# Optimization experiments

Hardware: AMD Instinct MI355X
Metric: run time of the kernel (lower is better)

Reference implementation:

```python
import jax, jax.numpy as jnp
import numpy as np
from jax import lax

STRIDES = (8, 16, 32, 64, 128)
LEVEL_HW = ((100, 128), (50, 64), (25, 32), (13, 16), (7, 8))
NUM_CLASSES = 80
PRE_NMS_THRESH = 0.05
PRE_NMS_TOPK = 1000
NMS_THRESH = 0.6
MAX_DET = 100
CLS_OFFSET = 1.0e4  # > max image coordinate, separates classes for joint NMS


def setup_inputs() -> dict:
    key = jax.random.key(0)
    B = 16
    ks = jax.random.split(key, 3 * len(LEVEL_HW))
    inp = {}
    i = 0
    for lvl, (h, w) in enumerate(LEVEL_HW):
        # shift logits down so sigmoid scores are mostly below the 0.05 candidate
        # threshold (realistic detection sparsity)
        inp[f"logits_p{lvl + 3}"] = jax.random.normal(ks[i], (B, NUM_CLASSES, h, w), jnp.float32) - 4.0; i += 1
        inp[f"bbox_p{lvl + 3}"] = jax.random.uniform(ks[i], (B, 4, h, w), jnp.float32, minval=0.0, maxval=64.0); i += 1
        inp[f"ctr_p{lvl + 3}"] = jax.random.normal(ks[i], (B, 1, h, w), jnp.float32); i += 1
    inp["im_info"] = jnp.tile(jnp.array([[800.0, 1024.0]], jnp.float32), (B, 1))
    return inp


def _locations(h, w, stride):
    # FCOSLocation: center of each stride cell -> [HW, 2] as (x, y)
    sx = jnp.arange(w, dtype=jnp.float32) * stride + stride // 2
    sy = jnp.arange(h, dtype=jnp.float32) * stride + stride // 2
    yy, xx = jnp.meshgrid(sy, sx, indexing="ij")
    return jnp.stack([xx.reshape(-1), yy.reshape(-1)], axis=-1)


def _nms_single(boxes, scores, classes):
    # boxes [K,4], scores [K] (descending), classes [K] int
    off = classes.astype(jnp.float32)[:, None] * CLS_OFFSET
    nb = boxes + off  # class-offset trick -> per-class NMS in one pass
    areas = jnp.maximum(nb[:, 2] - nb[:, 0], 0.0) * jnp.maximum(nb[:, 3] - nb[:, 1], 0.0)

    def body(sc, _):
        i = jnp.argmax(sc)
        s = sc[i]
        bi = nb[i]
        xx1 = jnp.maximum(bi[0], nb[:, 0])
        yy1 = jnp.maximum(bi[1], nb[:, 1])
        xx2 = jnp.minimum(bi[2], nb[:, 2])
        yy2 = jnp.minimum(bi[3], nb[:, 3])
        inter = jnp.maximum(xx2 - xx1, 0.0) * jnp.maximum(yy2 - yy1, 0.0)
        iou = inter / (areas[i] + areas - inter + 1e-9)
        sc2 = jnp.where(iou >= NMS_THRESH, -jnp.inf, sc).at[i].set(-jnp.inf)
        return sc2, (i, s > 0.0)

    _, (idxs, valid) = lax.scan(body, scores, None, length=MAX_DET)
    det = jnp.concatenate(
        [boxes[idxs], scores[idxs][:, None], classes[idxs].astype(jnp.float32)[:, None]],
        axis=-1,
    )  # [MAX_DET, 6] = x1,y1,x2,y2,score,class
    return jnp.where(valid[:, None], det, 0.0)


def _forward(logits_p3, bbox_p3, ctr_p3, logits_p4, bbox_p4, ctr_p4,
             logits_p5, bbox_p5, ctr_p5, logits_p6, bbox_p6, ctr_p6,
             logits_p7, bbox_p7, ctr_p7, im_info):
    levels = [(logits_p3, bbox_p3, ctr_p3), (logits_p4, bbox_p4, ctr_p4),
              (logits_p5, bbox_p5, ctr_p5), (logits_p6, bbox_p6, ctr_p6),
              (logits_p7, bbox_p7, ctr_p7)]
    scores_l, boxes_l = [], []
    for (lg, rg, ct), stride in zip(levels, STRIDES):
        B, C, H, W = lg.shape
        cls = jax.nn.sigmoid(lg).transpose(0, 2, 3, 1).reshape(B, H * W, C)
        cen = jax.nn.sigmoid(ct).transpose(0, 2, 3, 1).reshape(B, H * W, 1)
        # candidate threshold on raw class prob, then modulate by centerness
        comb = jnp.where(cls > PRE_NMS_THRESH, cls * cen, 0.0)
        locs = _locations(H, W, stride)  # [HW, 2]
        reg = rg.transpose(0, 2, 3, 1).reshape(B, H * W, 4)  # (l, t, r, b)
        bx = jnp.stack([locs[None, :, 0] - reg[..., 0],
                        locs[None, :, 1] - reg[..., 1],
                        locs[None, :, 0] + reg[..., 2],
                        locs[None, :, 1] + reg[..., 3]], axis=-1)
        scores_l.append(comb)
        boxes_l.append(bx)
    scores = jnp.concatenate(scores_l, axis=1)  # [B, N, C]
    boxes = jnp.concatenate(boxes_l, axis=1)    # [B, N, 4]
    B, N, C = scores.shape
    vals, idx = lax.top_k(scores.reshape(B, N * C), PRE_NMS_TOPK)  # [B, K]
    loc = idx // C
    cls_id = idx % C
    cand = jnp.take_along_axis(boxes, loc[..., None], axis=1)  # [B, K, 4]
    h = im_info[:, 0:1]
    w = im_info[:, 1:2]
    x1 = jnp.clip(cand[..., 0], 0.0, w - 1.0)
    y1 = jnp.clip(cand[..., 1], 0.0, h - 1.0)
    x2 = jnp.clip(cand[..., 2], 0.0, w - 1.0)
    y2 = jnp.clip(cand[..., 3], 0.0, h - 1.0)
    cand = jnp.stack([x1, y1, x2, y2], axis=-1)
    sc = jnp.where(vals > 0.0, jnp.sqrt(jnp.maximum(vals, 0.0) + 1e-12), 0.0)
    return jax.vmap(_nms_single)(cand, sc, cls_id)  # [B, MAX_DET, 6]


def reference(logits_p3, bbox_p3, ctr_p3, logits_p4, bbox_p4, ctr_p4,
              logits_p5, bbox_p5, ctr_p5, logits_p6, bbox_p6, ctr_p6,
              logits_p7, bbox_p7, ctr_p7, im_info):
    return _forward(logits_p3, bbox_p3, ctr_p3, logits_p4, bbox_p4, ctr_p4,
                    logits_p5, bbox_p5, ctr_p5, logits_p6, bbox_p6, ctr_p6,
                    logits_p7, bbox_p7, ctr_p7, im_info)
```

## Files before the change

kernel.cpp:

```cpp
#include <hip/hip_runtime.h>
#include <math.h>

#pragma clang fp contract(off)

#define NB 16
#define NC 80
#define NTOT 17064
#define TOPK 1000
#define NBINS 8192
#define CAP 4096
#define MAXDET 100
#define NREP 4
#define CNTSTRIDE 64
#define CHUNK 128
#define G1 128
#define NSEG 512
#define SEGW 512

struct Ptrs {
    const float* lg[5];
    const float* bb[5];
    const float* ct[5];
};

__device__ __forceinline__ void level_of(int n, int& l, int& hw, int& W,
                                         int& stride, int& half, int& HW) {
    if (n < 12800)      { l = 0; hw = n;         W = 128; stride = 8;   half = 4;  HW = 12800; }
    else if (n < 16000) { l = 1; hw = n - 12800; W = 64;  stride = 16;  half = 8;  HW = 3200;  }
    else if (n < 16800) { l = 2; hw = n - 16000; W = 32;  stride = 32;  half = 16; HW = 800;   }
    else if (n < 17008) { l = 3; hw = n - 16800; W = 16;  stride = 64;  half = 32; HW = 208;   }
    else                { l = 4; hw = n - 17008; W = 8;   stride = 128; half = 64; HW = 56;    }
}

__device__ __forceinline__ float fast_sig(float x) {
    float e = __expf(-x);
    return __builtin_amdgcn_rcpf(1.0f + e);
}

template<int HW4, int NF4, int LVOFF>
__device__ __forceinline__ void scan_level(const float* lgb, const float* ctb,
        int tid, int lane, int bx, int gx, unsigned FB_LO,
        unsigned long long* segp, unsigned& cur, unsigned long long ltmask) {
    for (int i0 = bx * 256; i0 < NF4; i0 += gx * 256) {
        int i = i0 + tid;
        bool f0 = false, f1 = false, f2 = false, f3 = false;
        unsigned long long k0 = 0, k1 = 0, k2 = 0, k3 = 0;
        if (i < NF4) {
            int c   = i / HW4;
            int hwf = i - c * HW4;
            float4 v = *(const float4*)(lgb + c * (HW4 * 4) + hwf * 4);
            if (v.x > -2.47f || v.y > -2.47f || v.z > -2.47f || v.w > -2.47f) {
                float4 cv = *(const float4*)(ctb + hwf * 4);
                int nbase = LVOFF + hwf * 4;
#define DO_J(J, X, CT, F, K)                                                  \
                if ((X) > -2.47f) {                                           \
                    float cls = fast_sig(X);                                  \
                    float cen = fast_sig(CT);                                 \
                    unsigned bits = __float_as_uint(cls * cen);               \
                    if (bits >= FB_LO) {                                      \
                        unsigned idx = (unsigned)((nbase + (J)) * NC + c);    \
                        K = ((unsigned long long)bits << 32) |                \
                            (0xFFFFFFFFu - idx);                              \
                        F = true;                                             \
                    }                                                         \
                }
                DO_J(0, v.x, cv.x, f0, k0)
                DO_J(1, v.y, cv.y, f1, k1)
                DO_J(2, v.z, cv.z, f2, k2)
                DO_J(3, v.w, cv.w, f3, k3)
#undef DO_J
            }
        }
        unsigned long long m0 = __ballot(f0), m1 = __ballot(f1);
        unsigned long long m2 = __ballot(f2), m3 = __ballot(f3);
        if ((m0 | m1 | m2 | m3) == 0ULL) continue;
        unsigned t0 = (unsigned)__popcll(m0), t1 = (unsigned)__popcll(m1);
        unsigned t2 = (unsigned)__popcll(m2), t3 = (unsigned)__popcll(m3);
        if (f0) { unsigned pos = cur + (unsigned)__popcll(m0 & ltmask);                if (pos < SEGW) segp[pos] = k0; }
        if (f1) { unsigned pos = cur + t0 + (unsigned)__popcll(m1 & ltmask);           if (pos < SEGW) segp[pos] = k1; }
        if (f2) { unsigned pos = cur + t0 + t1 + (unsigned)__popcll(m2 & ltmask);      if (pos < SEGW) segp[pos] = k2; }
        if (f3) { unsigned pos = cur + t0 + t1 + t2 + (unsigned)__popcll(m3 & ltmask); if (pos < SEGW) segp[pos] = k3; }
        cur += t0 + t1 + t2 + t3;
    }
}

__global__ void __launch_bounds__(256) k_scoreF(Ptrs p, unsigned* segcnt,
                                                unsigned long long* segbuf,
                                                unsigned* cnt2) {
    int b = blockIdx.y, tid = threadIdx.x, bx = blockIdx.x, gx = gridDim.x;
    int lane = tid & 63, wv = tid >> 6;
    if (bx == 0 && tid == 0) cnt2[(size_t)b * CNTSTRIDE] = 0;
    unsigned long long ltmask = (1ULL << lane) - 1ULL;
    unsigned FB_LO = __float_as_uint(0.08f) - 64u;
    unsigned long long* segp = segbuf + (((size_t)b * G1 + bx) * 4 + wv) * SEGW;
    unsigned cur = 0;

    scan_level<3200, 256000,     0>(p.lg[0] + (size_t)b * NC * 12800, p.ct[0] + (size_t)b * 12800, tid, lane, bx, gx, FB_LO, segp, cur, ltmask);
    scan_level< 800,  64000, 12800>(p.lg[1] + (size_t)b * NC * 3200,  p.ct[1] + (size_t)b * 3200,  tid, lane, bx, gx, FB_LO, segp, cur, ltmask);
    scan_level< 200,  16000, 16000>(p.lg[2] + (size_t)b * NC * 800,   p.ct[2] + (size_t)b * 800,   tid, lane, bx, gx, FB_LO, segp, cur, ltmask);
    scan_level<  52,   4160, 16800>(p.lg[3] + (size_t)b * NC * 208,   p.ct[3] + (size_t)b * 208,   tid, lane, bx, gx, FB_LO, segp, cur, ltmask);
    scan_level<  14,   1120, 17008>(p.lg[4] + (size_t)b * NC * 56,    p.ct[4] + (size_t)b * 56,    tid, lane, bx, gx, FB_LO, segp, cur, ltmask);

    if (lane == 0) segcnt[(size_t)b * NSEG + bx * 4 + wv] = cur;
}

template<int HW4, int NF4>
__device__ __forceinline__ void histf_level(const float* lgb, const float* ctb,
                                            int tid, unsigned* hist) {
    for (int i0 = 0; i0 < NF4; i0 += 1024) {
        int i = i0 + tid;
        if (i < NF4) {
            int c   = i / HW4;
            int hwf = i - c * HW4;
            float4 v = *(const float4*)(lgb + c * (HW4 * 4) + hwf * 4);
            if (v.x > -2.95f || v.y > -2.95f || v.z > -2.95f || v.w > -2.95f) {
                float4 cv = *(const float4*)(ctb + hwf * 4);
                float xs[4] = {v.x, v.y, v.z, v.w};
                float cs[4] = {cv.x, cv.y, cv.z, cv.w};
#pragma unroll
                for (int j = 0; j < 4; ++j) {
                    float x = xs[j];
                    if (x > -2.95f) {
                        float cls = fast_sig(x);
                        if (cls > 0.04999f) {
                            bool in = true;
                            if (cls < 0.05001f)
                                in = (1.0f / (1.0f + expf(-x))) > 0.05f;
                            if (in) {
                                float cen = fast_sig(cs[j]);
                                unsigned bits = __float_as_uint(cls * cen);
                                unsigned cb = (bits > 32u) ? bits - 32u : 0u;
                                atomicAdd(&hist[cb >> 19], 1u);
                            }
                        }
                    }
                }
            }
        }
    }
}

__global__ void __launch_bounds__(1024) k_threshF(Ptrs p, const unsigned* segcnt,
                                                  const unsigned long long* segbuf,
                                                  unsigned* T, unsigned* okf) {
    __shared__ unsigned hist[NBINS];
    __shared__ unsigned wred[16], wtot[16];
    __shared__ int s_flags;
    __shared__ int Tf;
    int b = blockIdx.x, tid = threadIdx.x, lane = tid & 63, wv = tid >> 6;
    if (tid == 0) { s_flags = 0; Tf = 0; }
    for (int i = tid; i < NBINS; i += 1024) hist[i] = 0;
    __syncthreads();

    bool ovf = false;
    for (int sg = wv; sg < NSEG; sg += 16) {
        unsigned cnt = segcnt[(size_t)b * NSEG + sg];
        if (cnt > SEGW) { ovf = true; cnt = SEGW; }
        const unsigned long long* src = segbuf + ((size_t)b * NSEG + sg) * SEGW;
        for (int i = lane; i < (int)cnt; i += 64) {
            unsigned bits = (unsigned)(src[i] >> 32);
            unsigned cb = (bits > 32u) ? bits - 32u : 0u;
            atomicAdd(&hist[cb >> 19], 1u);
        }
    }
    if (ovf) atomicOr(&s_flags, 1);
    __syncthreads();

    const unsigned B0 = __float_as_uint(0.08f);
    const int OKBIN = (int)(B0 >> 19) + 1;
    int base = tid * 8;
    unsigned okp = 0;
#pragma unroll
    for (int i = 0; i < 8; ++i) if (base + i >= OKBIN) okp += hist[base + i];
    for (int off = 32; off > 0; off >>= 1) okp += __shfl_down(okp, off);
    if (lane == 0) wred[wv] = okp;
    __syncthreads();
    if (tid == 0) {
        unsigned tot = 0;
        for (int w = 0; w < 16; ++w) tot += wred[w];
        if ((s_flags & 1) || tot < TOPK) atomicOr(&s_flags, 2);
    }
    __syncthreads();

    if (s_flags & 2) {
        for (int i = tid; i < NBINS; i += 1024) hist[i] = 0;
        __syncthreads();
        histf_level<3200, 256000>(p.lg[0] + (size_t)b * NC * 12800, p.ct[0] + (size_t)b * 12800, tid, hist);
        histf_level< 800,  64000>(p.lg[1] + (size_t)b * NC * 3200,  p.ct[1] + (size_t)b * 3200,  tid, hist);
        histf_level< 200,  16000>(p.lg[2] + (size_t)b * NC * 800,   p.ct[2] + (size_t)b * 800,   tid, hist);
        histf_level<  52,   4160>(p.lg[3] + (size_t)b * NC * 208,   p.ct[3] + (size_t)b * 208,   tid, hist);
        histf_level<  14,   1120>(p.lg[4] + (size_t)b * NC * 56,    p.ct[4] + (size_t)b * 56,    tid, hist);
        __syncthreads();
    }

    unsigned mysum = 0;
#pragma unroll
    for (int i = 0; i < 8; ++i) mysum += hist[base + i];
    unsigned incl = mysum;
#pragma unroll
    for (int off = 1; off < 64; off <<= 1) {
        unsigned v = __shfl_down(incl, off);
        if (lane + off < 64) incl += v;
    }
    if (lane == 0) wtot[wv] = incl;
    __syncthreads();
    unsigned above = 0;
    for (int w = wv + 1; w < 16; ++w) above += wtot[w];
    unsigned sufincl = incl + above;
    unsigned excl = sufincl - mysum;
    if (excl < TOPK && sufincl >= TOPK) {
        unsigned running = excl;
        for (int bin = base + 7; bin >= base; --bin) {
            running += hist[bin];
            if (running >= TOPK) { Tf = bin; break; }
        }
    }
    __syncthreads();
    if (tid == 0) { T[b] = (unsigned)Tf; okf[b] = (s_flags & 2) ? 0u : 1u; }
}

template<int HW4, int NF4, int LVOFF>
__device__ __forceinline__ void compact_level(const float* lgb, const float* ctb,
        int tid, int lane, int bx, int gx, unsigned Tb, float xpre,
        unsigned* cntb, unsigned long long* selb, unsigned long long ltmask) {
    for (int i0 = bx * 256; i0 < NF4; i0 += gx * 256) {
        int i = i0 + tid;
        bool f0 = false, f1 = false, f2 = false, f3 = false;
        unsigned long long k0 = 0, k1 = 0, k2 = 0, k3 = 0;
        if (i < NF4) {
            int c   = i / HW4;
            int hwf = i - c * HW4;
            float4 v = *(const float4*)(lgb + c * (HW4 * 4) + hwf * 4);
            if (v.x > xpre || v.y > xpre || v.z > xpre || v.w > xpre) {
                float4 cv = *(const float4*)(ctb + hwf * 4);
                int nbase = LVOFF + hwf * 4;
#define DO_J(J, X, CT, F, K)                                                  \
                if ((X) > xpre) {                                             \
                    float cls = 1.0f / (1.0f + expf(-(X)));                   \
                    if (cls > 0.05f) {                                        \
                        float cen = 1.0f / (1.0f + expf(-(CT)));              \
                        float comb = cls * cen;                               \
                        unsigned bits = __float_as_uint(comb);                \
                        if ((bits >> 19) >= Tb) {                             \
                            unsigned idx = (unsigned)((nbase + (J)) * NC + c);\
                            K = ((unsigned long long)bits << 32) |            \
                                (0xFFFFFFFFu - idx);                          \
                            F = true;                                         \
                        }                                                     \
                    }                                                         \
                }
                DO_J(0, v.x, cv.x, f0, k0)
                DO_J(1, v.y, cv.y, f1, k1)
                DO_J(2, v.z, cv.z, f2, k2)
                DO_J(3, v.w, cv.w, f3, k3)
#undef DO_J
            }
        }
        unsigned long long m0 = __ballot(f0), m1 = __ballot(f1);
        unsigned long long m2 = __ballot(f2), m3 = __ballot(f3);
        if ((m0 | m1 | m2 | m3) == 0ULL) continue;
        unsigned t0 = (unsigned)__popcll(m0), t1 = (unsigned)__popcll(m1);
        unsigned t2 = (unsigned)__popcll(m2), t3 = (unsigned)__popcll(m3);
        unsigned total = t0 + t1 + t2 + t3;
        int basep = 0;
        if (lane == 0) basep = (int)atomicAdd(cntb, total);
        basep = __shfl(basep, 0);
        if (f0) { int pos = basep + (int)__popcll(m0 & ltmask);                       if (pos < CAP) selb[pos] = k0; }
        if (f1) { int pos = basep + (int)t0 + (int)__popcll(m1 & ltmask);             if (pos < CAP) selb[pos] = k1; }
        if (f2) { int pos = basep + (int)(t0 + t1) + (int)__popcll(m2 & ltmask);      if (pos < CAP) selb[pos] = k2; }
        if (f3) { int pos = basep + (int)(t0 + t1 + t2) + (int)__popcll(m3 & ltmask); if (pos < CAP) selb[pos] = k3; }
    }
}

__global__ void __launch_bounds__(256) k_filterF(Ptrs p, const unsigned* T,
                                                 const unsigned* okf,
                                                 const unsigned* segcnt,
                                                 const unsigned long long* segbuf,
                                                 unsigned* cnt2, unsigned long long* sel) {
    int b = blockIdx.y, tid = threadIdx.x, lane = tid & 63;
    int bx = blockIdx.x, gx = gridDim.x;
    unsigned Tb = T[b];
    unsigned long long ltmask = (1ULL << lane) - 1ULL;
    unsigned* cntb = cnt2 + (size_t)b * CNTSTRIDE;
    unsigned long long* selb = sel + (size_t)b * CAP;

    if (okf[b]) {
        unsigned Tshift = Tb << 19;
        unsigned fmin = (Tshift >= 32u) ? Tshift - 32u : 0u;
        int per = NSEG / gx;
        for (int sg = bx * per; sg < bx * per + per; ++sg) {
            unsigned sc = segcnt[(size_t)b * NSEG + sg];
            if (sc > SEGW) sc = SEGW;
            const unsigned long long* src = segbuf + ((size_t)b * NSEG + sg) * SEGW;
            for (int i = tid; i < (int)sc; i += 256) {
                unsigned long long e = src[i];
                bool f = false;
                unsigned long long key = 0;
                if ((unsigned)(e >> 32) >= fmin) {
                    unsigned idx = 0xFFFFFFFFu - (unsigned)(e & 0xFFFFFFFFu);
                    int n = idx / NC, c = idx - n * NC;
                    int l, hw, W, stride, half, HW;
                    level_of(n, l, hw, W, stride, half, HW);
                    float x  = p.lg[l][(size_t)b * NC * HW + (size_t)c * HW + hw];
                    float ct = p.ct[l][(size_t)b * HW + hw];
                    float cls = 1.0f / (1.0f + expf(-x));
                    if (cls > 0.05f) {
                        float cen = 1.0f / (1.0f + expf(-ct));
                        unsigned be = __float_as_uint(cls * cen);
                        if ((be >> 19) >= Tb) {
                            key = ((unsigned long long)be << 32) | (e & 0xFFFFFFFFULL);
                            f = true;
                        }
                    }
                }
                unsigned long long mk = __ballot(f);
                if (mk) {
                    unsigned nw = (unsigned)__popcll(mk);
                    int basep = 0;
                    if (lane == 0) basep = (int)atomicAdd(cntb, nw);
                    basep = __shfl(basep, 0);
                    if (f) {
                        int pos = basep + (int)__popcll(mk & ltmask);
                        if (pos < CAP) selb[pos] = key;
                    }
                }
            }
        }
    } else {
        float mthr = __uint_as_float(Tb << 19);
        float xpre = -2.95f;
        if (mthr > 1e-37f && mthr < 1.0f) {
            float lm = logf(mthr / (1.0f - mthr)) - 0.01f;
            if (lm > xpre) xpre = lm;
        }
        compact_level<3200, 256000,     0>(p.lg[0] + (size_t)b * NC * 12800, p.ct[0] + (size_t)b * 12800, tid, lane, bx, gx, Tb, xpre, cntb, selb, ltmask);
        compact_level< 800,  64000, 12800>(p.lg[1] + (size_t)b * NC * 3200,  p.ct[1] + (size_t)b * 3200,  tid, lane, bx, gx, Tb, xpre, cntb, selb, ltmask);
        compact_level< 200,  16000, 16000>(p.lg[2] + (size_t)b * NC * 800,   p.ct[2] + (size_t)b * 800,   tid, lane, bx, gx, Tb, xpre, cntb, selb, ltmask);
        compact_level<  52,   4160, 16800>(p.lg[3] + (size_t)b * NC * 208,   p.ct[3] + (size_t)b * 208,   tid, lane, bx, gx, Tb, xpre, cntb, selb, ltmask);
        compact_level<  14,   1120, 17008>(p.lg[4] + (size_t)b * NC * 56,    p.ct[4] + (size_t)b * 56,    tid, lane, bx, gx, Tb, xpre, cntb, selb, ltmask);
    }
}

template<int HW4, int NF4>
__device__ __forceinline__ void hist_level(const float* lgb, const float* ctb,
                                           int tid, int bx, int gx, unsigned* lh) {
    for (int i0 = bx * 256; i0 < NF4; i0 += gx * 256) {
        int i = i0 + tid;
        if (i < NF4) {
            int c   = i / HW4;
            int hwf = i - c * HW4;
            float4 v  = *(const float4*)(lgb + c * (HW4 * 4) + hwf * 4);
            if (v.x > -2.95f || v.y > -2.95f || v.z > -2.95f || v.w > -2.95f) {
                float4 cv = *(const float4*)(ctb + hwf * 4);
                float xs[4] = {v.x, v.y, v.z, v.w};
                float cs[4] = {cv.x, cv.y, cv.z, cv.w};
#pragma unroll
                for (int j = 0; j < 4; ++j) {
                    float x = xs[j];
                    if (x > -2.95f) {
                        float cls = fast_sig(x);
                        if (cls > 0.04999f) {
                            bool in = true;
                            if (cls < 0.05001f)
                                in = (1.0f / (1.0f + expf(-x))) > 0.05f;
                            if (in) {
                                float cen = fast_sig(cs[j]);
                                unsigned bits = __float_as_uint(cls * cen);
                                unsigned cb = (bits > 32u) ? bits - 32u : 0u;
                                atomicAdd(&lh[cb >> 19], 1u);
                            }
                        }
                    }
                }
            }
        }
    }
}

__global__ void __launch_bounds__(256) k_histA(Ptrs p, unsigned* hist) {
    __shared__ unsigned lh[NBINS];
    int b = blockIdx.y, tid = threadIdx.x, bx = blockIdx.x, gx = gridDim.x;
    for (int i = tid; i < NBINS; i += 256) lh[i] = 0;
    __syncthreads();
    hist_level<3200, 256000>(p.lg[0] + (size_t)b * NC * 12800, p.ct[0] + (size_t)b * 12800, tid, bx, gx, lh);
    hist_level< 800,  64000>(p.lg[1] + (size_t)b * NC * 3200,  p.ct[1] + (size_t)b * 3200,  tid, bx, gx, lh);
    hist_level< 200,  16000>(p.lg[2] + (size_t)b * NC * 800,   p.ct[2] + (size_t)b * 800,   tid, bx, gx, lh);
    hist_level<  52,   4160>(p.lg[3] + (size_t)b * NC * 208,   p.ct[3] + (size_t)b * 208,   tid, bx, gx, lh);
    hist_level<  14,   1120>(p.lg[4] + (size_t)b * NC * 56,    p.ct[4] + (size_t)b * 56,    tid, bx, gx, lh);
    __syncthreads();
    unsigned* h = hist + ((size_t)(bx & (NREP - 1)) * NB + b) * NBINS;
    for (int i = tid; i < NBINS; i += 256) {
        unsigned v = lh[i];
        if (v) atomicAdd(&h[i], v);
    }
}

__global__ void __launch_bounds__(256) k_thresh(const unsigned* hist, unsigned* T) {
    __shared__ unsigned hl[NBINS];
    __shared__ unsigned wtot[4];
    __shared__ int Tf;
    int b = blockIdx.x, tid = threadIdx.x, lane = tid & 63, wv = tid >> 6;
    if (tid == 0) Tf = 0;
    for (int i = tid; i < NBINS; i += 256) {
        unsigned s = 0;
        for (int r = 0; r < NREP; ++r)
            s += hist[((size_t)r * NB + b) * NBINS + i];
        hl[i] = s;
    }
    __syncthreads();
    int base = tid * 32;
    unsigned mysum = 0;
#pragma unroll
    for (int i = 0; i < 32; ++i) mysum += hl[base + i];
    unsigned incl = mysum;
#pragma unroll
    for (int off = 1; off < 64; off <<= 1) {
        unsigned v = __shfl_down(incl, off);
        if (lane + off < 64) incl += v;
    }
    if (lane == 0) wtot[wv] = incl;
    __syncthreads();
    unsigned above = 0;
    for (int w = wv + 1; w < 4; ++w) above += wtot[w];
    unsigned sufincl = incl + above;
    unsigned excl = sufincl - mysum;
    if (excl < TOPK && sufincl >= TOPK) {
        unsigned running = excl;
        for (int bin = base + 31; bin >= base; --bin) {
            running += hl[bin];
            if (running >= TOPK) { Tf = bin; break; }
        }
    }
    __syncthreads();
    if (tid == 0) T[b] = (unsigned)Tf;
}

__global__ void __launch_bounds__(256) k_compactB(Ptrs p, const unsigned* T,
                                                  unsigned* cnt2, unsigned long long* sel) {
    int b = blockIdx.y, tid = threadIdx.x, lane = tid & 63;
    int bx = blockIdx.x, gx = gridDim.x;
    unsigned Tb = T[b];
    float mthr = __uint_as_float(Tb << 19);
    float xpre = -2.95f;
    if (mthr > 1e-37f && mthr < 1.0f) {
        float lm = logf(mthr / (1.0f - mthr)) - 0.01f;
        if (lm > xpre) xpre = lm;
    }
    unsigned long long ltmask = (1ULL << lane) - 1ULL;
    unsigned* cntb = cnt2 + (size_t)b * CNTSTRIDE;
    unsigned long long* selb = sel + (size_t)b * CAP;
    compact_level<3200, 256000,     0>(p.lg[0] + (size_t)b * NC * 12800, p.ct[0] + (size_t)b * 12800, tid, lane, bx, gx, Tb, xpre, cntb, selb, ltmask);
    compact_level< 800,  64000, 12800>(p.lg[1] + (size_t)b * NC * 3200,  p.ct[1] + (size_t)b * 3200,  tid, lane, bx, gx, Tb, xpre, cntb, selb, ltmask);
    compact_level< 200,  16000, 16000>(p.lg[2] + (size_t)b * NC * 800,   p.ct[2] + (size_t)b * 800,   tid, lane, bx, gx, Tb, xpre, cntb, selb, ltmask);
    compact_level<  52,   4160, 16800>(p.lg[3] + (size_t)b * NC * 208,   p.ct[3] + (size_t)b * 208,   tid, lane, bx, gx, Tb, xpre, cntb, selb, ltmask);
    compact_level<  14,   1120, 17008>(p.lg[4] + (size_t)b * NC * 56,    p.ct[4] + (size_t)b * 56,    tid, lane, bx, gx, Tb, xpre, cntb, selb, ltmask);
}

__global__ void __launch_bounds__(256) k_rankdec(Ptrs p, const unsigned* cnt,
                                                 const unsigned long long* sel,
                                                 const float* im_info, float* cand) {
    __shared__ __align__(16) unsigned long long keys[CAP];
    int b = blockIdx.y, tid = threadIdx.x;
    unsigned M = cnt[(size_t)b * CNTSTRIDE];
    if (M > CAP) M = CAP;
    int s0 = blockIdx.x * 256;
    if (s0 >= (int)M) return;
    int Mpad = (int)((M + 1u) & ~1u);
    for (int i = tid; i < Mpad; i += 256)
        keys[i] = (i < (int)M) ? sel[(size_t)b * CAP + i] : 0ULL;
    __syncthreads();

    int s = s0 + tid;
    if (s >= (int)M) return;
    unsigned long long k = keys[s];
    int rank = 0;
    for (int j = 0; j < Mpad; j += 2) {
        ulonglong2 kk = *(const ulonglong2*)&keys[j];
        rank += (kk.x > k) ? 1 : 0;
        rank += (kk.y > k) ? 1 : 0;
    }
    if (rank >= TOPK) return;

    float Him = im_info[b * 2 + 0], Wim = im_info[b * 2 + 1];
    float xmax = Wim - 1.0f, ymax = Him - 1.0f;
    unsigned sb = (unsigned)(k >> 32);
    unsigned idx = 0xFFFFFFFFu - (unsigned)(k & 0xFFFFFFFFu);
    float val = __uint_as_float(sb);
    int n = idx / NC, c = idx - n * NC;
    int l, hw, W, stride, half, HW;
    level_of(n, l, hw, W, stride, half, HW);
    int wx = hw % W, hy = hw / W;
    float locx = (float)(wx * stride + half);
    float locy = (float)(hy * stride + half);
    const float* bb = p.bb[l] + (size_t)b * 4 * HW + hw;
    float r0 = bb[0], r1 = bb[(size_t)HW], r2 = bb[(size_t)2 * HW], r3 = bb[(size_t)3 * HW];
    float x1 = locx - r0, y1 = locy - r1, x2 = locx + r2, y2 = locy + r3;
    x1 = fminf(fmaxf(x1, 0.f), xmax);
    y1 = fminf(fmaxf(y1, 0.f), ymax);
    x2 = fminf(fmaxf(x2, 0.f), xmax);
    y2 = fminf(fmaxf(y2, 0.f), ymax);
    float scv = sqrtf(val + 1e-12f);
    float off = (float)c * 10000.0f;
    float a0 = x1 + off, a1 = y1 + off, a2 = x2 + off, a3 = y2 + off;
    float area = fmaxf(a2 - a0, 0.f) * fmaxf(a3 - a1, 0.f);
    float* dst = cand + ((size_t)b * TOPK + rank) * 12;
    *(float4*)(dst + 0) = make_float4(x1, y1, x2, y2);
    *(float4*)(dst + 4) = make_float4(a0, a1, a2, a3);
    *(float4*)(dst + 8) = make_float4(area, scv, (float)c, 0.f);
}

__global__ void __launch_bounds__(64) k_nms(const unsigned* cnt, const float* cand,
                                            float* out) {
    __shared__ float4 s_ob[CHUNK], s_nb[CHUNK], s_ms[CHUNK];
    int b = blockIdx.x, lane = threadIdx.x;
    unsigned M = cnt[(size_t)b * CNTSTRIDE];
    if (M > CAP) M = CAP;
    int ncand = (int)M < TOPK ? (int)M : TOPK;
    const float* src = cand + (size_t)b * TOPK * 12;
    float* ob = out + (size_t)b * MAXDET * 6;

    int na = 0;
    float4 a0b = make_float4(0.f, 0.f, 0.f, 0.f);
    float4 a1b = make_float4(0.f, 0.f, 0.f, 0.f);
    float a0a = 0.f, a1a = 0.f;

    for (int base = 0; base < ncand && na < MAXDET; base += CHUNK) {
        int cn = ncand - base; if (cn > CHUNK) cn = CHUNK;
        for (int cidx = lane; cidx < cn; cidx += 64) {
            const float* s = src + (size_t)(base + cidx) * 12;
            s_ob[cidx] = *(const float4*)(s + 0);
            s_nb[cidx] = *(const float4*)(s + 4);
            s_ms[cidx] = *(const float4*)(s + 8);
        }
        __syncthreads();
        for (int r = 0; r < cn && na < MAXDET; ++r) {
            float4 cb = s_nb[r];
            float ca = s_ms[r].x;
            bool sup = false;
            if (lane < na) {
                float xx1 = fmaxf(a0b.x, cb.x);
                float yy1 = fmaxf(a0b.y, cb.y);
                float xx2 = fminf(a0b.z, cb.z);
                float yy2 = fminf(a0b.w, cb.w);
                float inter = fmaxf(xx2 - xx1, 0.f) * fmaxf(yy2 - yy1, 0.f);
                float iou = inter / (((a0a + ca) - inter) + 1e-9f);
                sup = (iou >= 0.6f);
            }
            if (lane + 64 < na) {
                float xx1 = fmaxf(a1b.x, cb.x);
                float yy1 = fmaxf(a1b.y, cb.y);
                float xx2 = fminf(a1b.z, cb.z);
                float yy2 = fminf(a1b.w, cb.w);
                float inter = fmaxf(xx2 - xx1, 0.f) * fmaxf(yy2 - yy1, 0.f);
                float iou = inter / (((a1a + ca) - inter) + 1e-9f);
                sup |= (iou >= 0.6f);
            }
            if (__ballot(sup) == 0ULL) {
                if (lane == (na & 63)) {
                    if (na < 64) { a0b = cb; a0a = ca; }
                    else         { a1b = cb; a1a = ca; }
                }
                if (lane == 0) {
                    float4 o4 = s_ob[r]; float4 m4 = s_ms[r];
                    ob[na * 6 + 0] = o4.x; ob[na * 6 + 1] = o4.y;
                    ob[na * 6 + 2] = o4.z; ob[na * 6 + 3] = o4.w;
                    ob[na * 6 + 4] = m4.y; ob[na * 6 + 5] = m4.z;
                }
                ++na;
            }
        }
        __syncthreads();
    }
    for (int q = na * 6 + lane; q < MAXDET * 6; q += 64)
        ob[q] = 0.f;
}

extern "C" void kernel_launch(void* const* d_in, const int* in_sizes, int n_in,
                              void* d_out, int out_size, void* d_ws, size_t ws_size,
                              hipStream_t stream) {
    Ptrs p;
    for (int l = 0; l < 5; ++l) {
        p.lg[l] = (const float*)d_in[3 * l + 0];
        p.bb[l] = (const float*)d_in[3 * l + 1];
        p.ct[l] = (const float*)d_in[3 * l + 2];
    }
    const float* im_info = (const float*)d_in[15];
    float* out = (float*)d_out;
    unsigned char* w = (unsigned char*)d_ws;

    if (ws_size >= (size_t)34884096) {
        unsigned* segcnt           = (unsigned*)(w);
        unsigned* cnt2             = (unsigned*)(w + 32768);
        unsigned* T                = (unsigned*)(w + 36864);
        unsigned* okf              = (unsigned*)(w + 37120);
        unsigned long long* sel    = (unsigned long long*)(w + 37376);
        float* cand                = (float*)(w + 561664);
        unsigned long long* segbuf = (unsigned long long*)(w + 1329664);

        k_scoreF<<<dim3(G1, NB), 256, 0, stream>>>(p, segcnt, segbuf, cnt2);
        k_threshF<<<NB, 1024, 0, stream>>>(p, segcnt, segbuf, T, okf);
        k_filterF<<<dim3(32, NB), 256, 0, stream>>>(p, T, okf, segcnt, segbuf, cnt2, sel);
        k_rankdec<<<dim3(16, NB), 256, 0, stream>>>(p, cnt2, sel, im_info, cand);
        k_nms<<<NB, 64, 0, stream>>>(cnt2, cand, out);
    } else {
        unsigned* hist          = (unsigned*)(w);
        unsigned* cnt2          = (unsigned*)(w + 2097152);
        unsigned* T             = (unsigned*)(w + 2101248);
        unsigned long long* sel = (unsigned long long*)(w + 2101504);
        float* cand             = (float*)(w + 2625792);

        hipMemsetAsync(w, 0, 2101504, stream);
        k_histA<<<dim3(64, NB), 256, 0, stream>>>(p, hist);
        k_thresh<<<NB, 256, 0, stream>>>(hist, T);
        k_compactB<<<dim3(128, NB), 256, 0, stream>>>(p, T, cnt2, sel);
        k_rankdec<<<dim3(16, NB), 256, 0, stream>>>(p, cnt2, sel, im_info, cand);
        k_nms<<<NB, 64, 0, stream>>>(cnt2, cand, out);
    }
}
```

Baseline: 277.1 us.

## Fuse threshold and filter kernels into single per-image pick kernel

```diff
diff --git a/kernel.cpp b/kernel.cpp
--- a/kernel.cpp
+++ b/kernel.cpp
@@ -85,11 +85,9 @@
 }
 
 __global__ void __launch_bounds__(256) k_scoreF(Ptrs p, unsigned* segcnt,
-                                                unsigned long long* segbuf,
-                                                unsigned* cnt2) {
+                                                unsigned long long* segbuf) {
     int b = blockIdx.y, tid = threadIdx.x, bx = blockIdx.x, gx = gridDim.x;
     int lane = tid & 63, wv = tid >> 6;
-    if (bx == 0 && tid == 0) cnt2[(size_t)b * CNTSTRIDE] = 0;
     unsigned long long ltmask = (1ULL << lane) - 1ULL;
     unsigned FB_LO = __float_as_uint(0.08f) - 64u;
     unsigned long long* segp = segbuf + (((size_t)b * G1 + bx) * 4 + wv) * SEGW;
@@ -140,85 +138,6 @@
     }
 }
 
-__global__ void __launch_bounds__(1024) k_threshF(Ptrs p, const unsigned* segcnt,
-                                                  const unsigned long long* segbuf,
-                                                  unsigned* T, unsigned* okf) {
-    __shared__ unsigned hist[NBINS];
-    __shared__ unsigned wred[16], wtot[16];
-    __shared__ int s_flags;
-    __shared__ int Tf;
-    int b = blockIdx.x, tid = threadIdx.x, lane = tid & 63, wv = tid >> 6;
-    if (tid == 0) { s_flags = 0; Tf = 0; }
-    for (int i = tid; i < NBINS; i += 1024) hist[i] = 0;
-    __syncthreads();
-
-    bool ovf = false;
-    for (int sg = wv; sg < NSEG; sg += 16) {
-        unsigned cnt = segcnt[(size_t)b * NSEG + sg];
-        if (cnt > SEGW) { ovf = true; cnt = SEGW; }
-        const unsigned long long* src = segbuf + ((size_t)b * NSEG + sg) * SEGW;
-        for (int i = lane; i < (int)cnt; i += 64) {
-            unsigned bits = (unsigned)(src[i] >> 32);
-            unsigned cb = (bits > 32u) ? bits - 32u : 0u;
-            atomicAdd(&hist[cb >> 19], 1u);
-        }
-    }
-    if (ovf) atomicOr(&s_flags, 1);
-    __syncthreads();
-
-    const unsigned B0 = __float_as_uint(0.08f);
-    const int OKBIN = (int)(B0 >> 19) + 1;
-    int base = tid * 8;
-    unsigned okp = 0;
-#pragma unroll
-    for (int i = 0; i < 8; ++i) if (base + i >= OKBIN) okp += hist[base + i];
-    for (int off = 32; off > 0; off >>= 1) okp += __shfl_down(okp, off);
-    if (lane == 0) wred[wv] = okp;
-    __syncthreads();
-    if (tid == 0) {
-        unsigned tot = 0;
-        for (int w = 0; w < 16; ++w) tot += wred[w];
-        if ((s_flags & 1) || tot < TOPK) atomicOr(&s_flags, 2);
-    }
-    __syncthreads();
-
-    if (s_flags & 2) {
-        for (int i = tid; i < NBINS; i += 1024) hist[i] = 0;
-        __syncthreads();
-        histf_level<3200, 256000>(p.lg[0] + (size_t)b * NC * 12800, p.ct[0] + (size_t)b * 12800, tid, hist);
-        histf_level< 800,  64000>(p.lg[1] + (size_t)b * NC * 3200,  p.ct[1] + (size_t)b * 3200,  tid, hist);
-        histf_level< 200,  16000>(p.lg[2] + (size_t)b * NC * 800,   p.ct[2] + (size_t)b * 800,   tid, hist);
-        histf_level<  52,   4160>(p.lg[3] + (size_t)b * NC * 208,   p.ct[3] + (size_t)b * 208,   tid, hist);
-        histf_level<  14,   1120>(p.lg[4] + (size_t)b * NC * 56,    p.ct[4] + (size_t)b * 56,    tid, hist);
-        __syncthreads();
-    }
-
-    unsigned mysum = 0;
-#pragma unroll
-    for (int i = 0; i < 8; ++i) mysum += hist[base + i];
-    unsigned incl = mysum;
-#pragma unroll
-    for (int off = 1; off < 64; off <<= 1) {
-        unsigned v = __shfl_down(incl, off);
-        if (lane + off < 64) incl += v;
-    }
-    if (lane == 0) wtot[wv] = incl;
-    __syncthreads();
-    unsigned above = 0;
-    for (int w = wv + 1; w < 16; ++w) above += wtot[w];
-    unsigned sufincl = incl + above;
-    unsigned excl = sufincl - mysum;
-    if (excl < TOPK && sufincl >= TOPK) {
-        unsigned running = excl;
-        for (int bin = base + 7; bin >= base; --bin) {
-            running += hist[bin];
-            if (running >= TOPK) { Tf = bin; break; }
-        }
-    }
-    __syncthreads();
-    if (tid == 0) { T[b] = (unsigned)Tf; okf[b] = (s_flags & 2) ? 0u : 1u; }
-}
-
 template<int HW4, int NF4, int LVOFF>
 __device__ __forceinline__ void compact_level(const float* lgb, const float* ctb,
         int tid, int lane, int bx, int gx, unsigned Tb, float xpre,
@@ -272,44 +191,87 @@
     }
 }
 
-__global__ void __launch_bounds__(256) k_filterF(Ptrs p, const unsigned* T,
-                                                 const unsigned* okf,
-                                                 const unsigned* segcnt,
-                                                 const unsigned long long* segbuf,
-                                                 unsigned* cnt2, unsigned long long* sel) {
-    int b = blockIdx.y, tid = threadIdx.x, lane = tid & 63;
-    int bx = blockIdx.x, gx = gridDim.x;
-    unsigned Tb = T[b];
-    unsigned long long ltmask = (1ULL << lane) - 1ULL;
+__global__ void __launch_bounds__(1024) k_pick(Ptrs p, const unsigned* segcnt,
+                                               const unsigned long long* segbuf,
+                                               unsigned* cnt2, unsigned long long* sel) {
+    __shared__ unsigned wh[16][64];
+    __shared__ unsigned red[64];
+    __shared__ unsigned fullh[NBINS];
+    __shared__ int s_flags, s_T, s_ok;
+    int b = blockIdx.x, tid = threadIdx.x, lane = tid & 63, wv = tid >> 6;
+    if (tid == 0) { s_flags = 0; cnt2[(size_t)b * CNTSTRIDE] = 0; }
+    ((unsigned*)wh)[tid] = 0;
+    __syncthreads();
+
+    const int BINBASE = (int)(__float_as_uint(0.08f) >> 19);
+    bool ovf = false;
+    for (int sg = wv; sg < NSEG; sg += 16) {
+        unsigned cnt = segcnt[(size_t)b * NSEG + sg];
+        if (cnt > SEGW) { ovf = true; cnt = SEGW; }
+        const unsigned long long* src = segbuf + ((size_t)b * NSEG + sg) * SEGW;
+        for (int i = lane; i < (int)cnt; i += 64) {
+            unsigned bits = (unsigned)(src[i] >> 32);
+            unsigned cb = (bits > 32u) ? bits - 32u : 0u;
+            int lb = (int)(cb >> 19) - BINBASE;
+            lb = (lb < 0) ? 0 : ((lb > 63) ? 63 : lb);
+            atomicAdd(&wh[wv][lb], 1u);
+        }
+    }
+    if (ovf) atomicOr(&s_flags, 1);
+    __syncthreads();
+    if (tid < 64) {
+        unsigned s = 0;
+#pragma unroll
+        for (int w = 0; w < 16; ++w) s += wh[w][tid];
+        red[tid] = s;
+    }
+    __syncthreads();
+    if (tid == 0) {
+        unsigned total = 0;
+        for (int i = 0; i < 64; ++i) total += red[i];
+        unsigned suf1 = total - red[0];
+        unsigned run = 0; int Tl = 0;
+        for (int i = 63; i >= 0; --i) {
+            run += red[i];
+            if (run >= TOPK) { Tl = i; break; }
+        }
+        s_ok = ((s_flags & 1) == 0) && (suf1 >= TOPK);
+        s_T = Tl + BINBASE;
+    }
+    __syncthreads();
+
     unsigned* cntb = cnt2 + (size_t)b * CNTSTRIDE;
     unsigned long long* selb = sel + (size_t)b * CAP;
-
-    if (okf[b]) {
-        unsigned Tshift = Tb << 19;
-        unsigned fmin = (Tshift >= 32u) ? Tshift - 32u : 0u;
-        int per = NSEG / gx;
-        for (int sg = bx * per; sg < bx * per + per; ++sg) {
-            unsigned sc = segcnt[(size_t)b * NSEG + sg];
-            if (sc > SEGW) sc = SEGW;
+    unsigned long long ltmask = (1ULL << lane) - 1ULL;
+    unsigned Tb = (unsigned)s_T;
+
+    if (s_ok) {
+        unsigned fmin = (Tb << 19) - 32u;
+        for (int sg = wv; sg < NSEG; sg += 16) {
+            unsigned cnt = segcnt[(size_t)b * NSEG + sg];
+            if (cnt > SEGW) cnt = SEGW;
             const unsigned long long* src = segbuf + ((size_t)b * NSEG + sg) * SEGW;
-            for (int i = tid; i < (int)sc; i += 256) {
-                unsigned long long e = src[i];
+            for (unsigned i0 = 0; i0 < cnt; i0 += 64) {
+                unsigned i = i0 + (unsigned)lane;
                 bool f = false;
                 unsigned long long key = 0;
-                if ((unsigned)(e >> 32) >= fmin) {
-                    unsigned idx = 0xFFFFFFFFu - (unsigned)(e & 0xFFFFFFFFu);
-                    int n = idx / NC, c = idx - n * NC;
-                    int l, hw, W, stride, half, HW;
-                    level_of(n, l, hw, W, stride, half, HW);
-                    float x  = p.lg[l][(size_t)b * NC * HW + (size_t)c * HW + hw];
-                    float ct = p.ct[l][(size_t)b * HW + hw];
-                    float cls = 1.0f / (1.0f + expf(-x));
-                    if (cls > 0.05f) {
-                        float cen = 1.0f / (1.0f + expf(-ct));
-                        unsigned be = __float_as_uint(cls * cen);
-                        if ((be >> 19) >= Tb) {
-                            key = ((unsigned long long)be << 32) | (e & 0xFFFFFFFFULL);
-                            f = true;
+                if (i < cnt) {
+                    unsigned long long e = src[i];
+                    if ((unsigned)(e >> 32) >= fmin) {
+                        unsigned idx = 0xFFFFFFFFu - (unsigned)(e & 0xFFFFFFFFu);
+                        int n = idx / NC, c = idx - n * NC;
+                        int l, hw, W, stride, half, HW;
+                        level_of(n, l, hw, W, stride, half, HW);
+                        float x  = p.lg[l][(size_t)b * NC * HW + (size_t)c * HW + hw];
+                        float ct = p.ct[l][(size_t)b * HW + hw];
+                        float cls = 1.0f / (1.0f + expf(-x));
+                        if (cls > 0.05f) {
+                            float cen = 1.0f / (1.0f + expf(-ct));
+                            unsigned be = __float_as_uint(cls * cen);
+                            if ((be >> 19) >= Tb) {
+                                key = ((unsigned long long)be << 32) | (e & 0xFFFFFFFFULL);
+                                f = true;
+                            }
                         }
                     }
                 }
@@ -327,17 +289,36 @@
             }
         }
     } else {
+        for (int i = tid; i < NBINS; i += 1024) fullh[i] = 0;
+        __syncthreads();
+        histf_level<3200, 256000>(p.lg[0] + (size_t)b * NC * 12800, p.ct[0] + (size_t)b * 12800, tid, fullh);
+        histf_level< 800,  64000>(p.lg[1] + (size_t)b * NC * 3200,  p.ct[1] + (size_t)b * 3200,  tid, fullh);
+        histf_level< 200,  16000>(p.lg[2] + (size_t)b * NC * 800,   p.ct[2] + (size_t)b * 800,   tid, fullh);
+        histf_level<  52,   4160>(p.lg[3] + (size_t)b * NC * 208,   p.ct[3] + (size_t)b * 208,   tid, fullh);
+        histf_level<  14,   1120>(p.lg[4] + (size_t)b * NC * 56,    p.ct[4] + (size_t)b * 56,    tid, fullh);
+        __syncthreads();
+        if (tid == 0) {
+            unsigned run = 0; int Tf2 = 0;
+            for (int i = NBINS - 1; i >= 0; --i) {
+                run += fullh[i];
+                if (run >= TOPK) { Tf2 = i; break; }
+            }
+            s_T = Tf2;
+        }
+        __syncthreads();
+        Tb = (unsigned)s_T;
         float mthr = __uint_as_float(Tb << 19);
         float xpre = -2.95f;
         if (mthr > 1e-37f && mthr < 1.0f) {
             float lm = logf(mthr / (1.0f - mthr)) - 0.01f;
             if (lm > xpre) xpre = lm;
         }
-        compact_level<3200, 256000,     0>(p.lg[0] + (size_t)b * NC * 12800, p.ct[0] + (size_t)b * 12800, tid, lane, bx, gx, Tb, xpre, cntb, selb, ltmask);
-        compact_level< 800,  64000, 12800>(p.lg[1] + (size_t)b * NC * 3200,  p.ct[1] + (size_t)b * 3200,  tid, lane, bx, gx, Tb, xpre, cntb, selb, ltmask);
-        compact_level< 200,  16000, 16000>(p.lg[2] + (size_t)b * NC * 800,   p.ct[2] + (size_t)b * 800,   tid, lane, bx, gx, Tb, xpre, cntb, selb, ltmask);
-        compact_level<  52,   4160, 16800>(p.lg[3] + (size_t)b * NC * 208,   p.ct[3] + (size_t)b * 208,   tid, lane, bx, gx, Tb, xpre, cntb, selb, ltmask);
-        compact_level<  14,   1120, 17008>(p.lg[4] + (size_t)b * NC * 56,    p.ct[4] + (size_t)b * 56,    tid, lane, bx, gx, Tb, xpre, cntb, selb, ltmask);
+        int vbx = tid >> 8, vtid = tid & 255;
+        compact_level<3200, 256000,     0>(p.lg[0] + (size_t)b * NC * 12800, p.ct[0] + (size_t)b * 12800, vtid, lane, vbx, 4, Tb, xpre, cntb, selb, ltmask);
+        compact_level< 800,  64000, 12800>(p.lg[1] + (size_t)b * NC * 3200,  p.ct[1] + (size_t)b * 3200,  vtid, lane, vbx, 4, Tb, xpre, cntb, selb, ltmask);
+        compact_level< 200,  16000, 16000>(p.lg[2] + (size_t)b * NC * 800,   p.ct[2] + (size_t)b * 800,   vtid, lane, vbx, 4, Tb, xpre, cntb, selb, ltmask);
+        compact_level<  52,   4160, 16800>(p.lg[3] + (size_t)b * NC * 208,   p.ct[3] + (size_t)b * 208,   vtid, lane, vbx, 4, Tb, xpre, cntb, selb, ltmask);
+        compact_level<  14,   1120, 17008>(p.lg[4] + (size_t)b * NC * 56,    p.ct[4] + (size_t)b * 56,    vtid, lane, vbx, 4, Tb, xpre, cntb, selb, ltmask);
     }
 }
 
@@ -588,18 +569,15 @@
     float* out = (float*)d_out;
     unsigned char* w = (unsigned char*)d_ws;
 
-    if (ws_size >= (size_t)34884096) {
+    if (ws_size >= (size_t)34883584) {
         unsigned* segcnt           = (unsigned*)(w);
         unsigned* cnt2             = (unsigned*)(w + 32768);
-        unsigned* T                = (unsigned*)(w + 36864);
-        unsigned* okf              = (unsigned*)(w + 37120);
-        unsigned long long* sel    = (unsigned long long*)(w + 37376);
-        float* cand                = (float*)(w + 561664);
-        unsigned long long* segbuf = (unsigned long long*)(w + 1329664);
-
-        k_scoreF<<<dim3(G1, NB), 256, 0, stream>>>(p, segcnt, segbuf, cnt2);
-        k_threshF<<<NB, 1024, 0, stream>>>(p, segcnt, segbuf, T, okf);
-        k_filterF<<<dim3(32, NB), 256, 0, stream>>>(p, T, okf, segcnt, segbuf, cnt2, sel);
+        unsigned long long* sel    = (unsigned long long*)(w + 36864);
+        float* cand                = (float*)(w + 561152);
+        unsigned long long* segbuf = (unsigned long long*)(w + 1329152);
+
+        k_scoreF<<<dim3(G1, NB), 256, 0, stream>>>(p, segcnt, segbuf);
+        k_pick<<<NB, 1024, 0, stream>>>(p, segcnt, segbuf, cnt2, sel);
         k_rankdec<<<dim3(16, NB), 256, 0, stream>>>(p, cnt2, sel, im_info, cand);
         k_nms<<<NB, 64, 0, stream>>>(cnt2, cand, out);
     } else {
```

New measurement: 319.0 us. +15.1%, slower.
